# Kernel optimization log

Hardware: AMD Instinct MI355X
Metric: run time of the kernel (lower is better)

## Reference

```python
import jax, jax.numpy as jnp
import numpy as np

D = 768
NH = 8
HD = D // NH
DFF = 2048
EPS = 1e-5


def _layer_norm(x, g, b):
    mu = jnp.mean(x, axis=-1, keepdims=True)
    var = jnp.mean(jnp.square(x - mu), axis=-1, keepdims=True)
    return (x - mu) * jax.lax.rsqrt(var + EPS) * g + b


def setup_inputs() -> dict:
    key = jax.random.key(0)
    ks = jax.random.split(key, 16)
    B, L = 2, 2048
    s = 0.02
    return {
        "x": jax.random.normal(ks[0], (B, L, D), jnp.float32),
        "attn_bias": jax.random.normal(ks[1], (B, L, L), jnp.float32),
        "in_proj_w": jax.random.normal(ks[2], (3 * D, D), jnp.float32) * s,
        "in_proj_b": jnp.zeros((3 * D,), jnp.float32),
        "out_w": jax.random.normal(ks[3], (D, D), jnp.float32) * s,
        "out_b": jnp.zeros((D,), jnp.float32),
        "W1": jax.random.normal(ks[4], (DFF, D), jnp.float32) * s,
        "b1": jnp.zeros((DFF,), jnp.float32),
        "W2": jax.random.normal(ks[5], (D, DFF), jnp.float32) * s,
        "b2": jnp.zeros((D,), jnp.float32),
        "g1": jnp.ones((D,), jnp.float32),
        "be1": jnp.zeros((D,), jnp.float32),
        "g2": jnp.ones((D,), jnp.float32),
        "be2": jnp.zeros((D,), jnp.float32),
    }


def reference(x, attn_bias, in_proj_w, in_proj_b, out_w, out_b,
              W1, b1, W2, b2, g1, be1, g2, be2):
    B, L, _ = x.shape
    # fused qkv projection (torch nn.MultiheadAttention in_proj)
    qkv = x @ in_proj_w.T + in_proj_b          # [B, L, 3D]
    q, k, v = jnp.split(qkv, 3, axis=-1)
    q = q.reshape(B, L, NH, HD).transpose(0, 2, 1, 3)  # [B, nH, L, hd]
    k = k.reshape(B, L, NH, HD).transpose(0, 2, 1, 3)
    v = v.reshape(B, L, NH, HD).transpose(0, 2, 1, 3)
    scale = 1.0 / jnp.sqrt(jnp.asarray(HD, x.dtype))
    scores = jnp.einsum("bhqd,bhkd->bhqk", q * scale, k)
    scores = scores + attn_bias[:, None, :, :]         # broadcast over heads == expand
    attn = jax.nn.softmax(scores, axis=-1)
    ctx = jnp.einsum("bhqk,bhkd->bhqd", attn, v)       # [B, nH, L, hd]
    ctx = ctx.transpose(0, 2, 1, 3).reshape(B, L, D)
    attn_out = ctx @ out_w.T + out_b
    x = _layer_norm(x + attn_out, g1, be1)
    h = jax.nn.gelu(x @ W1.T + b1, approximate=False)  # torch default GELU = erf
    ff = h @ W2.T + b2
    return _layer_norm(x + ff, g2, be2)
```

## Files before the change

### kernel.cpp

```cpp
#include <hip/hip_runtime.h>
#include <hip/hip_bf16.h>
#include <math.h>

typedef __bf16 bf16;
typedef __attribute__((ext_vector_type(8))) __bf16 bf16x8;
typedef __attribute__((ext_vector_type(4))) __bf16 bf16x4;
typedef __attribute__((ext_vector_type(2))) __bf16 bf16x2;
typedef __attribute__((ext_vector_type(4))) float f32x4;

#define LOG2E 1.4426950408889634f

__device__ __forceinline__ void gload16(const bf16* g, bf16* l) {
  __builtin_amdgcn_global_load_lds(
      (const __attribute__((address_space(1))) void*)g,
      (__attribute__((address_space(3))) void*)l, 16, 0, 0);
}

__device__ __forceinline__ unsigned packbf2(float a, float b) {
  bf16x2 v = { (bf16)a, (bf16)b };
  return __builtin_bit_cast(unsigned, v);
}

__device__ __forceinline__ int xcd_swz(int id, int nwg) {
  return (id & 7) * (nwg >> 3) + (id >> 3);
}

struct CastSegs { const float* src[5]; bf16* dst[5]; };

__global__ void fused_cast_kernel(CastSegs segs) {
  const int e0 = 786432, e1 = 1228800, e2 = 1376256, e3 = 1769472, e4 = 2162688;
  int i = blockIdx.x * blockDim.x + threadIdx.x;
  int stride = gridDim.x * blockDim.x;
  for (; i < e4; i += stride) {
    int s = 0, base = 0;
    if (i >= e0) { s = 1; base = e0; }
    if (i >= e1) { s = 2; base = e1; }
    if (i >= e2) { s = 3; base = e2; }
    if (i >= e3) { s = 4; base = e3; }
    float4 v = ((const float4*)segs.src[s])[i - base];
    bf16x4 o = { (bf16)v.x, (bf16)v.y, (bf16)v.z, (bf16)v.w };
    ((bf16x4*)segs.dst[s])[i - base] = o;
  }
}

template<int MODE>
__launch_bounds__(256)
__global__ void gemm_kernel(const bf16* __restrict__ A, const bf16* __restrict__ W,
                            const float* __restrict__ bias, bf16* __restrict__ vt,
                            void* __restrict__ out, int K, int O) {
  __shared__ bf16 As[128 * 64];
  __shared__ bf16 Bs[128 * 64];
  const int gx = gridDim.x;
  const int id = blockIdx.y * gx + blockIdx.x;
  const int swz = xcd_swz(id, gx * gridDim.y);
  const int n0 = (swz / gx) * 128;
  const int o0 = (swz % gx) * 128;
  const int t    = threadIdx.x;
  const int lane = t & 63;
  const int wave = t >> 6;
  const int wr = (wave >> 1) * 64;
  const int wc = (wave & 1) * 64;

  f32x4 zero = {0.f, 0.f, 0.f, 0.f};
  f32x4 acc[4][4];
#pragma unroll
  for (int m = 0; m < 4; m++)
#pragma unroll
    for (int n = 0; n < 4; n++) acc[m][n] = zero;

  const int fr  = lane & 15;
  const int fg8 = (lane >> 4) * 8;

  for (int k0 = 0; k0 < K; k0 += 64) {
    __syncthreads();
#pragma unroll
    for (int c = 0; c < 4; c++) {
      int f = c * 256 + t;
      int row = f >> 3;
      int col = (f & 7) * 8;
      gload16(&A[(size_t)(n0 + row) * K + k0 + col], &As[f * 8]);
      gload16(&W[(size_t)(o0 + row) * K + k0 + col], &Bs[f * 8]);
    }
    __syncthreads();
#pragma unroll
    for (int kf = 0; kf < 2; kf++) {
      bf16x8 a[4], b[4];
#pragma unroll
      for (int m = 0; m < 4; m++) a[m] = *(const bf16x8*)&As[(wr + m * 16 + fr) * 64 + kf * 32 + fg8];
#pragma unroll
      for (int n = 0; n < 4; n++) b[n] = *(const bf16x8*)&Bs[(wc + n * 16 + fr) * 64 + kf * 32 + fg8];
#pragma unroll
      for (int m = 0; m < 4; m++)
#pragma unroll
        for (int n = 0; n < 4; n++)
          acc[m][n] = __builtin_amdgcn_mfma_f32_16x16x32_bf16(a[m], b[n], acc[m][n], 0, 0, 0);
    }
  }

  const int fg4 = (lane >> 4) * 4;
#pragma unroll
  for (int m = 0; m < 4; m++) {
#pragma unroll
    for (int n = 0; n < 4; n++) {
      int col = o0 + wc + n * 16 + fr;
      float bv = bias[col];
      if constexpr (MODE == 3) {
        if (col >= 1536) {
          int c = col - 1536;
          int h = c / 96;
          int hd = c - h * 96;
          int row0 = n0 + wr + m * 16 + fg4;
          int b = row0 >> 11;
          int token = row0 & 2047;
          bf16x4 ov;
#pragma unroll
          for (int r = 0; r < 4; r++) ov[r] = (bf16)(acc[m][n][r] + bv);
          *(bf16x4*)&vt[((size_t)((b * 8 + h) * 96 + hd)) * 2048 + token] = ov;
          continue;
        }
      }
#pragma unroll
      for (int r = 0; r < 4; r++) {
        int row = n0 + wr + m * 16 + fg4 + r;
        float v = acc[m][n][r] + bv;
        if constexpr (MODE == 2) {
          v = 0.5f * v * (1.0f + erff(v * 0.70710678118654752f));
          ((bf16*)out)[(size_t)row * O + col] = (bf16)v;
        } else {
          ((bf16*)out)[(size_t)row * O + col] = (bf16)v;
        }
      }
    }
  }
}

__launch_bounds__(256)
__global__ void gemmSK_kernel(const bf16* __restrict__ A, const bf16* __restrict__ W,
                              float* __restrict__ out, int K, int O) {
  __shared__ bf16 As[128 * 64];
  __shared__ bf16 Bs[128 * 64];
  const int gx = gridDim.x;
  const int id = blockIdx.y * gx + blockIdx.x;
  const int swz = xcd_swz(id, gx * gridDim.y);
  const int n0 = (swz / gx) * 128;
  const int o0 = (swz % gx) * 128;
  const int t    = threadIdx.x;
  const int lane = t & 63;
  const int wave = t >> 6;
  const int wr = (wave >> 1) * 64;
  const int wc = (wave & 1) * 64;
  const int khalf = K >> 1;
  const int kbeg = blockIdx.z * khalf;

  f32x4 zero = {0.f, 0.f, 0.f, 0.f};
  f32x4 acc[4][4];
#pragma unroll
  for (int m = 0; m < 4; m++)
#pragma unroll
    for (int n = 0; n < 4; n++) acc[m][n] = zero;

  const int fr  = lane & 15;
  const int fg8 = (lane >> 4) * 8;

  for (int k0 = kbeg; k0 < kbeg + khalf; k0 += 64) {
    __syncthreads();
#pragma unroll
    for (int c = 0; c < 4; c++) {
      int f = c * 256 + t;
      int row = f >> 3;
      int col = (f & 7) * 8;
      gload16(&A[(size_t)(n0 + row) * K + k0 + col], &As[f * 8]);
      gload16(&W[(size_t)(o0 + row) * K + k0 + col], &Bs[f * 8]);
    }
    __syncthreads();
#pragma unroll
    for (int kf = 0; kf < 2; kf++) {
      bf16x8 a[4], b[4];
#pragma unroll
      for (int m = 0; m < 4; m++) a[m] = *(const bf16x8*)&As[(wr + m * 16 + fr) * 64 + kf * 32 + fg8];
#pragma unroll
      for (int n = 0; n < 4; n++) b[n] = *(const bf16x8*)&Bs[(wc + n * 16 + fr) * 64 + kf * 32 + fg8];
#pragma unroll
      for (int m = 0; m < 4; m++)
#pragma unroll
        for (int n = 0; n < 4; n++)
          acc[m][n] = __builtin_amdgcn_mfma_f32_16x16x32_bf16(a[m], b[n], acc[m][n], 0, 0, 0);
    }
  }

  float* op = out + (size_t)blockIdx.z * 4096 * O;
  const int fg4 = (lane >> 4) * 4;
#pragma unroll
  for (int m = 0; m < 4; m++) {
#pragma unroll
    for (int n = 0; n < 4; n++) {
      int col = o0 + wc + n * 16 + fr;
#pragma unroll
      for (int r = 0; r < 4; r++) {
        int row = n0 + wr + m * 16 + fg4 + r;
        op[(size_t)row * O + col] = acc[m][n][r];
      }
    }
  }
}

__launch_bounds__(256, 4)
__global__ void attn_kernel(const bf16* __restrict__ qkv, const bf16* __restrict__ vt,
                            const float* __restrict__ bias, float* __restrict__ opart,
                            float* __restrict__ ml) {
  __shared__ bf16 Ks[64 * 96];
  __shared__ bf16 Vs[96 * 64];
  const int t    = threadIdx.x;
  const int lane = t & 63;
  const int wave = t >> 6;
  const int bid = blockIdx.x;
  const int xcd = bid & 7, j = bid >> 3;
  const int h = j & 7;
  const int g_ = xcd * 16 + (j >> 3);
  const int qb = g_ & 31;
  const int bh = g_ >> 5;
  const int half = bh & 1, b = bh >> 1;
  const int kvstart = half * 1024;
  const int q0 = qb * 64 + wave * 16;
  const int fq = lane & 15;
  const int g  = lane >> 4;
  const size_t base = (size_t)b * 2048 * 2304;

  bf16x8 qf[3];
  {
    const bf16* qp = qkv + base + (size_t)(q0 + fq) * 2304 + h * 96;
#pragma unroll
    for (int f = 0; f < 3; f++) qf[f] = *(const bf16x8*)(qp + f * 32 + g * 8);
  }

  const int krow = t >> 2, kg = t & 3;
  const int ksw = kg ^ (krow & 3);
  const int vrow0 = t >> 3, vc = t & 7;
  const int vsw = vc ^ (vrow0 & 7);
  const bf16* kbase = qkv + base + (size_t)kvstart * 2304 + 768 + h * 96;
  const bf16* vbase = vt + (size_t)((b * 8 + h) * 96) * 2048 + kvstart;

  bf16x8 kreg[3], vreg[3];
#pragma unroll
  for (int i = 0; i < 3; i++) {
    kreg[i] = *(const bf16x8*)(kbase + (size_t)krow * 2304 + i * 32 + kg * 8);
    vreg[i] = *(const bf16x8*)(vbase + (size_t)(vrow0 + 32 * i) * 2048 + vc * 8);
  }

  float l_run = 0.f;
  f32x4 zero = {0.f, 0.f, 0.f, 0.f};
  f32x4 o_acc[6];
#pragma unroll
  for (int i = 0; i < 6; i++) o_acc[i] = zero;

  const float scale = 0.10206207261596575f;
  const float* bp = bias + ((size_t)b * 2048 + q0 + fq) * 2048 + kvstart;

  const int krd = fq * 96 + (g ^ (fq & 3)) * 8;
  const int vrd0 = fq * 64 + ((0 * 4 + g) ^ (fq & 7)) * 8;
  const int vrd1 = fq * 64 + ((1 * 4 + g) ^ (fq & 7)) * 8;

  for (int kv0 = 0; kv0 < 1024; kv0 += 64) {
    if (kv0) __syncthreads();
#pragma unroll
    for (int i = 0; i < 3; i++) {
      *(bf16x8*)&Ks[(krow * 12 + i * 4 + ksw) * 8] = kreg[i];
      *(bf16x8*)&Vs[((vrow0 + 32 * i) * 8 + vsw) * 8] = vreg[i];
    }
    if (kv0 + 64 < 1024) {
      int nx = kv0 + 64;
#pragma unroll
      for (int i = 0; i < 3; i++) {
        kreg[i] = *(const bf16x8*)(kbase + (size_t)(nx + krow) * 2304 + i * 32 + kg * 8);
        vreg[i] = *(const bf16x8*)(vbase + (size_t)(vrow0 + 32 * i) * 2048 + nx + vc * 8);
      }
    }
    __builtin_amdgcn_sched_barrier(0);
    __syncthreads();

    float4 bfv[4];
#pragma unroll
    for (int kvt = 0; kvt < 4; kvt++)
      bfv[kvt] = *(const float4*)(bp + kv0 + kvt * 16 + g * 4);

    f32x4 s[4];
    __builtin_amdgcn_s_setprio(1);
#pragma unroll
    for (int kvt = 0; kvt < 4; kvt++) {
      s[kvt] = zero;
#pragma unroll
      for (int f = 0; f < 3; f++) {
        bf16x8 kfr = *(const bf16x8*)&Ks[kvt * 1536 + krd + f * 32];
        s[kvt] = __builtin_amdgcn_mfma_f32_16x16x32_bf16(kfr, qf[f], s[kvt], 0, 0, 0);
      }
    }
    __builtin_amdgcn_s_setprio(0);

    float rsum = 0.f;
    uint2 d[4];
#pragma unroll
    for (int kvt = 0; kvt < 4; kvt++) {
      float e0 = exp2f(fmaf(s[kvt][0], scale, (&bfv[kvt].x)[0]) * LOG2E);
      float e1 = exp2f(fmaf(s[kvt][1], scale, (&bfv[kvt].x)[1]) * LOG2E);
      float e2 = exp2f(fmaf(s[kvt][2], scale, (&bfv[kvt].x)[2]) * LOG2E);
      float e3 = exp2f(fmaf(s[kvt][3], scale, (&bfv[kvt].x)[3]) * LOG2E);
      rsum += (e0 + e1) + (e2 + e3);
      d[kvt].x = packbf2(e0, e1);
      d[kvt].y = packbf2(e2, e3);
    }
    rsum += __shfl_xor(rsum, 16);
    rsum += __shfl_xor(rsum, 32);
    l_run += rsum;

    bf16x8 pb[2];
    {
      bool glow = (g < 2);
      uint2 snd0 = glow ? d[1] : d[0];
      uint2 snd1 = glow ? d[3] : d[2];
      uint2 r0, r1;
      r0.x = __shfl_xor(snd0.x, 32); r0.y = __shfl_xor(snd0.y, 32);
      r1.x = __shfl_xor(snd1.x, 32); r1.y = __shfl_xor(snd1.y, 32);
      uint2 k0 = glow ? d[0] : d[1];
      uint2 k1 = glow ? d[2] : d[3];
      bool sendk = ((g ^ (g >> 1)) & 1);
      uint2 s0 = sendk ? k0 : r0;
      uint2 s1 = sendk ? k1 : r1;
      uint2 q0_, q1_;
      q0_.x = __shfl_xor(s0.x, 16); q0_.y = __shfl_xor(s0.y, 16);
      q1_.x = __shfl_xor(s1.x, 16); q1_.y = __shfl_xor(s1.y, 16);
      uint2 kept0 = sendk ? r0 : k0;
      uint2 kept1 = sendk ? r1 : k1;
      bool godd = (g & 1);
      uint2 lo0 = godd ? q0_ : kept0;
      uint2 hi0 = godd ? kept0 : q0_;
      uint2 lo1 = godd ? q1_ : kept1;
      uint2 hi1 = godd ? kept1 : q1_;
      uint4 u0 = { lo0.x, lo0.y, hi0.x, hi0.y };
      uint4 u1 = { lo1.x, lo1.y, hi1.x, hi1.y };
      pb[0] = __builtin_bit_cast(bf16x8, u0);
      pb[1] = __builtin_bit_cast(bf16x8, u1);
    }

    __builtin_amdgcn_s_setprio(1);
#pragma unroll
    for (int ht = 0; ht < 6; ht++) {
      bf16x8 v0 = *(const bf16x8*)&Vs[ht * 1024 + vrd0];
      o_acc[ht] = __builtin_amdgcn_mfma_f32_16x16x32_bf16(v0, pb[0], o_acc[ht], 0, 0, 0);
      bf16x8 v1 = *(const bf16x8*)&Vs[ht * 1024 + vrd1];
      o_acc[ht] = __builtin_amdgcn_mfma_f32_16x16x32_bf16(v1, pb[1], o_acc[ht], 0, 0, 0);
    }
    __builtin_amdgcn_s_setprio(0);
  }

  {
    int q = q0 + fq;
    float* op = opart + (size_t)half * (16 * 2048 * 96) + ((size_t)(b * 8 + h) * 2048 + q) * 96;
#pragma unroll
    for (int ht = 0; ht < 6; ht++)
      *(f32x4*)&op[ht * 16 + g * 4] = o_acc[ht];
    if (g == 0) ml[(size_t)half * 32768 + (size_t)(b * 8 + h) * 2048 + q] = l_run;
  }
}

__launch_bounds__(256)
__global__ void attn_combine_kernel(const float* __restrict__ opart, const float* __restrict__ ml,
                                    bf16* __restrict__ ctx) {
  int idx = blockIdx.x * blockDim.x + threadIdx.x;
  if (idx >= 786432) return;
  int e = idx * 4;
  int bh = e / (2048 * 96);
  int rem = e - bh * (2048 * 96);
  int q = rem / 96;
  int hd = rem - q * 96;
  const float* op0 = opart;
  const float* op1 = opart + (size_t)16 * 2048 * 96;
  float4 o1 = *(const float4*)&op0[e];
  float4 o2 = *(const float4*)&op1[e];
  float l1 = ml[(size_t)bh * 2048 + q];
  float l2 = ml[(size_t)32768 + (size_t)bh * 2048 + q];
  float inv = 1.0f / (l1 + l2);
  int b = bh >> 3, h = bh & 7;
  bf16x4 o;
  o[0] = (bf16)((o1.x + o2.x) * inv);
  o[1] = (bf16)((o1.y + o2.y) * inv);
  o[2] = (bf16)((o1.z + o2.z) * inv);
  o[3] = (bf16)((o1.w + o2.w) * inv);
  *(bf16x4*)&ctx[((size_t)b * 2048 + q) * 768 + h * 96 + hd] = o;
}

__launch_bounds__(256)
__global__ void lnf_kernel(const float* __restrict__ p0, const float* __restrict__ p1,
                           const float* __restrict__ bias, const float* __restrict__ res,
                           const float* __restrict__ gamma, const float* __restrict__ beta,
                           float* __restrict__ outf, bf16* __restrict__ outb) {
  const int row = blockIdx.x;
  const int t = threadIdx.x;
  const size_t off = (size_t)row * 768;
  float v[3];
#pragma unroll
  for (int i = 0; i < 3; i++) {
    int col = t + 256 * i;
    v[i] = p0[off + col] + p1[off + col] + bias[col] + res[off + col];
  }
  float s = v[0] + v[1] + v[2];
  float ss = v[0] * v[0] + v[1] * v[1] + v[2] * v[2];
#pragma unroll
  for (int o = 1; o < 64; o <<= 1) {
    s += __shfl_xor(s, o);
    ss += __shfl_xor(ss, o);
  }
  __shared__ float red[8];
  if ((t & 63) == 0) { red[(t >> 6) * 2] = s; red[(t >> 6) * 2 + 1] = ss; }
  __syncthreads();
  s = red[0] + red[2] + red[4] + red[6];
  ss = red[1] + red[3] + red[5] + red[7];
  float mu = s * (1.0f / 768.0f);
  float var = ss * (1.0f / 768.0f) - mu * mu;
  float rs = rsqrtf(var + 1e-5f);
#pragma unroll
  for (int i = 0; i < 3; i++) {
    int col = t + 256 * i;
    float y = (v[i] - mu) * rs * gamma[col] + beta[col];
    outf[off + col] = y;
    if (outb) outb[off + col] = (bf16)y;
  }
}

extern "C" void kernel_launch(void* const* d_in, const int* in_sizes, int n_in,
                              void* d_out, int out_size, void* d_ws, size_t ws_size,
                              hipStream_t stream) {
  (void)in_sizes; (void)n_in; (void)out_size; (void)ws_size;
  const float* x     = (const float*)d_in[0];
  const float* ab    = (const float*)d_in[1];
  const float* w_qkv = (const float*)d_in[2];
  const float* b_qkv = (const float*)d_in[3];
  const float* w_out = (const float*)d_in[4];
  const float* b_out = (const float*)d_in[5];
  const float* W1    = (const float*)d_in[6];
  const float* b1    = (const float*)d_in[7];
  const float* W2    = (const float*)d_in[8];
  const float* b2    = (const float*)d_in[9];
  const float* g1    = (const float*)d_in[10];
  const float* be1   = (const float*)d_in[11];
  const float* g2    = (const float*)d_in[12];
  const float* be2   = (const float*)d_in[13];
  float* outf = (float*)d_out;

  char* p = (char*)d_ws;
  bf16* xb    = (bf16*)p;  p += (size_t)4096 * 768 * 2;
  bf16* qkv   = (bf16*)p;  p += (size_t)4096 * 2304 * 2;
  bf16* ctx   = (bf16*)p;  p += (size_t)4096 * 768 * 2;
  float* x1f  = (float*)p; p += (size_t)4096 * 768 * 4;
  bf16* x1b   = (bf16*)p;  p += (size_t)4096 * 768 * 2;
  bf16* hbuf  = (bf16*)p;  p += (size_t)4096 * 2048 * 2;
  bf16* wqkvb = (bf16*)p;  p += (size_t)2304 * 768 * 2;
  bf16* woutb = (bf16*)p;  p += (size_t)768 * 768 * 2;
  bf16* w1b   = (bf16*)p;  p += (size_t)2048 * 768 * 2;
  bf16* w2b   = (bf16*)p;  p += (size_t)768 * 2048 * 2;
  float* opart = (float*)p; p += (size_t)2 * 16 * 2048 * 96 * 4;
  float* mlb   = (float*)p; p += (size_t)2 * 32768 * 4;
  bf16* vtb   = (bf16*)x1f;
  float* pSK  = opart;

  CastSegs segs;
  segs.src[0] = x;     segs.dst[0] = xb;
  segs.src[1] = w_qkv; segs.dst[1] = wqkvb;
  segs.src[2] = w_out; segs.dst[2] = woutb;
  segs.src[3] = W1;    segs.dst[3] = w1b;
  segs.src[4] = W2;    segs.dst[4] = w2b;
  fused_cast_kernel<<<2048, 256, 0, stream>>>(segs);

  gemm_kernel<3><<<dim3(18, 32), 256, 0, stream>>>(xb, wqkvb, b_qkv, vtb, qkv, 768, 2304);
  attn_kernel<<<1024, 256, 0, stream>>>(qkv, vtb, ab, opart, mlb);
  attn_combine_kernel<<<3072, 256, 0, stream>>>(opart, mlb, ctx);
  gemmSK_kernel<<<dim3(6, 32, 2), 256, 0, stream>>>(ctx, woutb, pSK, 768, 768);
  lnf_kernel<<<4096, 256, 0, stream>>>(pSK, pSK + (size_t)4096 * 768, b_out, x, g1, be1, x1f, x1b);
  gemm_kernel<2><<<dim3(16, 32), 256, 0, stream>>>(x1b, w1b, b1, nullptr, hbuf, 768, 2048);
  gemmSK_kernel<<<dim3(6, 32, 2), 256, 0, stream>>>(hbuf, w2b, pSK, 2048, 768);
  lnf_kernel<<<4096, 256, 0, stream>>>(pSK, pSK + (size_t)4096 * 768, b2, x1f, g2, be2, outf, nullptr);
}
```

Baseline: 212.9 us.

## Drop split-KV attention and combine kernel, normalize in-kernel with prefetched bias

The attention kernel now walks the full 2048-long KV range in a single block instead of splitting KV into two halves. This removes the fp32 partial outputs, the row-sum buffer and the separate combine kernel, and the block normalizes and writes bf16 context directly. The row-sum cross-lane reduction moves out of the loop to the end. The scale is folded together with LOG2E, the bias tile for the next step is prefetched and pre-multiplied, and cross-lane shuffles use permlane swap builtins where available. The cost is half as many blocks (512), which lowers parallelism and occupancy across CUs.

New measurement: 208.5 us (median of 2 runs). 1.02x faster.

```diff
diff --git a/kernel.cpp b/kernel.cpp
--- a/kernel.cpp
+++ b/kernel.cpp
@@ -7,6 +7,7 @@
 typedef __attribute__((ext_vector_type(4))) __bf16 bf16x4;
 typedef __attribute__((ext_vector_type(2))) __bf16 bf16x2;
 typedef __attribute__((ext_vector_type(4))) float f32x4;
+typedef __attribute__((ext_vector_type(2))) unsigned uint2v;
 
 #define LOG2E 1.4426950408889634f
 
@@ -19,6 +20,29 @@
 __device__ __forceinline__ unsigned packbf2(float a, float b) {
   bf16x2 v = { (bf16)a, (bf16)b };
   return __builtin_bit_cast(unsigned, v);
+}
+
+__device__ __forceinline__ unsigned shx32u(unsigned v) {
+#if __has_builtin(__builtin_amdgcn_permlane32_swap)
+  uint2v r = __builtin_amdgcn_permlane32_swap(v, v, false, false);
+  return (threadIdx.x & 32) ? r[0] : r[1];
+#else
+  return __shfl_xor(v, 32);
+#endif
+}
+__device__ __forceinline__ unsigned shx16u(unsigned v) {
+#if __has_builtin(__builtin_amdgcn_permlane16_swap)
+  uint2v r = __builtin_amdgcn_permlane16_swap(v, v, false, false);
+  return (threadIdx.x & 16) ? r[0] : r[1];
+#else
+  return __shfl_xor(v, 16);
+#endif
+}
+__device__ __forceinline__ float shx32f(float v) {
+  return __builtin_bit_cast(float, shx32u(__builtin_bit_cast(unsigned, v)));
+}
+__device__ __forceinline__ float shx16f(float v) {
+  return __builtin_bit_cast(float, shx16u(__builtin_bit_cast(unsigned, v)));
 }
 
 __device__ __forceinline__ int xcd_swz(int id, int nwg) {
@@ -206,8 +230,7 @@
 
 __launch_bounds__(256, 4)
 __global__ void attn_kernel(const bf16* __restrict__ qkv, const bf16* __restrict__ vt,
-                            const float* __restrict__ bias, float* __restrict__ opart,
-                            float* __restrict__ ml) {
+                            const float* __restrict__ bias, bf16* __restrict__ ctx) {
   __shared__ bf16 Ks[64 * 96];
   __shared__ bf16 Vs[96 * 64];
   const int t    = threadIdx.x;
@@ -216,11 +239,9 @@
   const int bid = blockIdx.x;
   const int xcd = bid & 7, j = bid >> 3;
   const int h = j & 7;
-  const int g_ = xcd * 16 + (j >> 3);
+  const int g_ = xcd * 8 + (j >> 3);
   const int qb = g_ & 31;
-  const int bh = g_ >> 5;
-  const int half = bh & 1, b = bh >> 1;
-  const int kvstart = half * 1024;
+  const int b  = g_ >> 5;
   const int q0 = qb * 64 + wave * 16;
   const int fq = lane & 15;
   const int g  = lane >> 4;
@@ -237,8 +258,8 @@
   const int ksw = kg ^ (krow & 3);
   const int vrow0 = t >> 3, vc = t & 7;
   const int vsw = vc ^ (vrow0 & 7);
-  const bf16* kbase = qkv + base + (size_t)kvstart * 2304 + 768 + h * 96;
-  const bf16* vbase = vt + (size_t)((b * 8 + h) * 96) * 2048 + kvstart;
+  const bf16* kbase = qkv + base + 768 + h * 96;
+  const bf16* vbase = vt + (size_t)((b * 8 + h) * 96) * 2048;
 
   bf16x8 kreg[3], vreg[3];
 #pragma unroll
@@ -253,21 +274,28 @@
 #pragma unroll
   for (int i = 0; i < 6; i++) o_acc[i] = zero;
 
-  const float scale = 0.10206207261596575f;
-  const float* bp = bias + ((size_t)b * 2048 + q0 + fq) * 2048 + kvstart;
+  const float scl2 = 0.10206207261596575f * LOG2E;
+  const float* bp = bias + ((size_t)b * 2048 + q0 + fq) * 2048;
+
+  float4 bfv[4];
+#pragma unroll
+  for (int kvt = 0; kvt < 4; kvt++) {
+    float4 bv = *(const float4*)(bp + kvt * 16 + g * 4);
+    bfv[kvt] = make_float4(bv.x * LOG2E, bv.y * LOG2E, bv.z * LOG2E, bv.w * LOG2E);
+  }
 
   const int krd = fq * 96 + (g ^ (fq & 3)) * 8;
   const int vrd0 = fq * 64 + ((0 * 4 + g) ^ (fq & 7)) * 8;
   const int vrd1 = fq * 64 + ((1 * 4 + g) ^ (fq & 7)) * 8;
 
-  for (int kv0 = 0; kv0 < 1024; kv0 += 64) {
+  for (int kv0 = 0; kv0 < 2048; kv0 += 64) {
     if (kv0) __syncthreads();
 #pragma unroll
     for (int i = 0; i < 3; i++) {
       *(bf16x8*)&Ks[(krow * 12 + i * 4 + ksw) * 8] = kreg[i];
       *(bf16x8*)&Vs[((vrow0 + 32 * i) * 8 + vsw) * 8] = vreg[i];
     }
-    if (kv0 + 64 < 1024) {
+    if (kv0 + 64 < 2048) {
       int nx = kv0 + 64;
 #pragma unroll
       for (int i = 0; i < 3; i++) {
@@ -278,11 +306,6 @@
     __builtin_amdgcn_sched_barrier(0);
     __syncthreads();
 
-    float4 bfv[4];
-#pragma unroll
-    for (int kvt = 0; kvt < 4; kvt++)
-      bfv[kvt] = *(const float4*)(bp + kv0 + kvt * 16 + g * 4);
-
     f32x4 s[4];
     __builtin_amdgcn_s_setprio(1);
 #pragma unroll
@@ -300,17 +323,24 @@
     uint2 d[4];
 #pragma unroll
     for (int kvt = 0; kvt < 4; kvt++) {
-      float e0 = exp2f(fmaf(s[kvt][0], scale, (&bfv[kvt].x)[0]) * LOG2E);
-      float e1 = exp2f(fmaf(s[kvt][1], scale, (&bfv[kvt].x)[1]) * LOG2E);
-      float e2 = exp2f(fmaf(s[kvt][2], scale, (&bfv[kvt].x)[2]) * LOG2E);
-      float e3 = exp2f(fmaf(s[kvt][3], scale, (&bfv[kvt].x)[3]) * LOG2E);
+      float e0 = exp2f(fmaf(s[kvt][0], scl2, (&bfv[kvt].x)[0]));
+      float e1 = exp2f(fmaf(s[kvt][1], scl2, (&bfv[kvt].x)[1]));
+      float e2 = exp2f(fmaf(s[kvt][2], scl2, (&bfv[kvt].x)[2]));
+      float e3 = exp2f(fmaf(s[kvt][3], scl2, (&bfv[kvt].x)[3]));
       rsum += (e0 + e1) + (e2 + e3);
       d[kvt].x = packbf2(e0, e1);
       d[kvt].y = packbf2(e2, e3);
     }
-    rsum += __shfl_xor(rsum, 16);
-    rsum += __shfl_xor(rsum, 32);
     l_run += rsum;
+
+    {
+      int nxb = (kv0 + 64) & 2047;
+#pragma unroll
+      for (int kvt = 0; kvt < 4; kvt++) {
+        float4 bv = *(const float4*)(bp + nxb + kvt * 16 + g * 4);
+        bfv[kvt] = make_float4(bv.x * LOG2E, bv.y * LOG2E, bv.z * LOG2E, bv.w * LOG2E);
+      }
+    }
 
     bf16x8 pb[2];
     {
@@ -318,16 +348,16 @@
       uint2 snd0 = glow ? d[1] : d[0];
       uint2 snd1 = glow ? d[3] : d[2];
       uint2 r0, r1;
-      r0.x = __shfl_xor(snd0.x, 32); r0.y = __shfl_xor(snd0.y, 32);
-      r1.x = __shfl_xor(snd1.x, 32); r1.y = __shfl_xor(snd1.y, 32);
+      r0.x = shx32u(snd0.x); r0.y = shx32u(snd0.y);
+      r1.x = shx32u(snd1.x); r1.y = shx32u(snd1.y);
       uint2 k0 = glow ? d[0] : d[1];
       uint2 k1 = glow ? d[2] : d[3];
       bool sendk = ((g ^ (g >> 1)) & 1);
       uint2 s0 = sendk ? k0 : r0;
       uint2 s1 = sendk ? k1 : r1;
       uint2 q0_, q1_;
-      q0_.x = __shfl_xor(s0.x, 16); q0_.y = __shfl_xor(s0.y, 16);
-      q1_.x = __shfl_xor(s1.x, 16); q1_.y = __shfl_xor(s1.y, 16);
+      q0_.x = shx16u(s0.x); q0_.y = shx16u(s0.y);
+      q1_.x = shx16u(s1.x); q1_.y = shx16u(s1.y);
       uint2 kept0 = sendk ? r0 : k0;
       uint2 kept1 = sendk ? r1 : k1;
       bool godd = (g & 1);
@@ -352,40 +382,17 @@
     __builtin_amdgcn_s_setprio(0);
   }
 
-  {
-    int q = q0 + fq;
-    float* op = opart + (size_t)half * (16 * 2048 * 96) + ((size_t)(b * 8 + h) * 2048 + q) * 96;
-#pragma unroll
-    for (int ht = 0; ht < 6; ht++)
-      *(f32x4*)&op[ht * 16 + g * 4] = o_acc[ht];
-    if (g == 0) ml[(size_t)half * 32768 + (size_t)(b * 8 + h) * 2048 + q] = l_run;
-  }
-}
-
-__launch_bounds__(256)
-__global__ void attn_combine_kernel(const float* __restrict__ opart, const float* __restrict__ ml,
-                                    bf16* __restrict__ ctx) {
-  int idx = blockIdx.x * blockDim.x + threadIdx.x;
-  if (idx >= 786432) return;
-  int e = idx * 4;
-  int bh = e / (2048 * 96);
-  int rem = e - bh * (2048 * 96);
-  int q = rem / 96;
-  int hd = rem - q * 96;
-  const float* op0 = opart;
-  const float* op1 = opart + (size_t)16 * 2048 * 96;
-  float4 o1 = *(const float4*)&op0[e];
-  float4 o2 = *(const float4*)&op1[e];
-  float l1 = ml[(size_t)bh * 2048 + q];
-  float l2 = ml[(size_t)32768 + (size_t)bh * 2048 + q];
-  float inv = 1.0f / (l1 + l2);
-  int b = bh >> 3, h = bh & 7;
-  bf16x4 o;
-  o[0] = (bf16)((o1.x + o2.x) * inv);
-  o[1] = (bf16)((o1.y + o2.y) * inv);
-  o[2] = (bf16)((o1.z + o2.z) * inv);
-  o[3] = (bf16)((o1.w + o2.w) * inv);
-  *(bf16x4*)&ctx[((size_t)b * 2048 + q) * 768 + h * 96 + hd] = o;
+  l_run += shx16f(l_run);
+  l_run += shx32f(l_run);
+  float inv = 1.0f / l_run;
+  bf16* cp = ctx + ((size_t)b * 2048 + q0 + fq) * 768 + h * 96;
+#pragma unroll
+  for (int ht = 0; ht < 6; ht++) {
+    bf16x4 ov;
+#pragma unroll
+    for (int r = 0; r < 4; r++) ov[r] = (bf16)(o_acc[ht][r] * inv);
+    *(bf16x4*)(cp + ht * 16 + g * 4) = ov;
+  }
 }
 
 __launch_bounds__(256)
@@ -457,10 +464,8 @@
   bf16* woutb = (bf16*)p;  p += (size_t)768 * 768 * 2;
   bf16* w1b   = (bf16*)p;  p += (size_t)2048 * 768 * 2;
   bf16* w2b   = (bf16*)p;  p += (size_t)768 * 2048 * 2;
-  float* opart = (float*)p; p += (size_t)2 * 16 * 2048 * 96 * 4;
-  float* mlb   = (float*)p; p += (size_t)2 * 32768 * 4;
+  float* pSK  = (float*)p; p += (size_t)2 * 4096 * 768 * 4;
   bf16* vtb   = (bf16*)x1f;
-  float* pSK  = opart;
 
   CastSegs segs;
   segs.src[0] = x;     segs.dst[0] = xb;
@@ -471,8 +476,7 @@
   fused_cast_kernel<<<2048, 256, 0, stream>>>(segs);
 
   gemm_kernel<3><<<dim3(18, 32), 256, 0, stream>>>(xb, wqkvb, b_qkv, vtb, qkv, 768, 2304);
-  attn_kernel<<<1024, 256, 0, stream>>>(qkv, vtb, ab, opart, mlb);
-  attn_combine_kernel<<<3072, 256, 0, stream>>>(opart, mlb, ctx);
+  attn_kernel<<<512, 256, 0, stream>>>(qkv, vtb, ab, ctx);
   gemmSK_kernel<<<dim3(6, 32, 2), 256, 0, stream>>>(ctx, woutb, pSK, 768, 768);
   lnf_kernel<<<4096, 256, 0, stream>>>(pSK, pSK + (size_t)4096 * 768, b_out, x, g1, be1, x1f, x1b);
   gemm_kernel<2><<<dim3(16, 32), 256, 0, stream>>>(x1b, w1b, b1, nullptr, hbuf, 768, 2048);
```
